# Performance work log

Hardware: AMD Instinct MI355X
Metric: run time of the kernel (lower is better)

The kernel has to match this reference:

```python
import jax, jax.numpy as jnp
import numpy as np

N_NODES = 50000
N_EDGES = 800000
IN_FEATS, HIDDEN, OUT = 256, 64, 32


def graph_conv(x, W, b, src, dst, n_nodes):
    # DGL GraphConv with norm='both': h = D_in^{-1/2} A D_out^{-1/2} (x W) + b
    ones = jnp.ones((src.shape[0],), dtype=x.dtype)
    deg_out = jax.ops.segment_sum(ones, src, num_segments=n_nodes)
    deg_in = jax.ops.segment_sum(ones, dst, num_segments=n_nodes)
    norm_out = jax.lax.rsqrt(jnp.maximum(deg_out, 1.0))  # [N]
    norm_in = jax.lax.rsqrt(jnp.maximum(deg_in, 1.0))    # [N]
    xw = x @ W                                # [N, out] dense transform first
    msg = (xw * norm_out[:, None])[src]       # [E, out] gather
    agg = jax.ops.segment_sum(msg, dst, num_segments=n_nodes)  # [N, out]
    return agg * norm_in[:, None] + b


def setup_inputs() -> dict:
    key = jax.random.key(0)
    ks = jax.random.split(key, 9)
    inputs = jax.random.normal(ks[0], (N_NODES, IN_FEATS), dtype=jnp.float32)
    src = jax.random.randint(ks[1], (N_EDGES,), 0, N_NODES)
    dst = jax.random.randint(ks[2], (N_EDGES,), 0, N_NODES)
    W1 = jax.random.normal(ks[3], (IN_FEATS, HIDDEN), dtype=jnp.float32) / np.sqrt(IN_FEATS)
    b1 = jnp.zeros((HIDDEN,), dtype=jnp.float32)
    W2 = jax.random.normal(ks[4], (HIDDEN, OUT), dtype=jnp.float32) / np.sqrt(HIDDEN)
    b2 = jnp.zeros((OUT,), dtype=jnp.float32)
    fc_w = jax.random.normal(ks[5], (N_NODES,), dtype=jnp.float32) / np.sqrt(N_NODES)
    fc_b = jnp.zeros((1,), dtype=jnp.float32)
    return {"inputs": inputs, "src": src, "dst": dst,
            "W1": W1, "b1": b1, "W2": W2, "b2": b2,
            "fc_w": fc_w, "fc_b": fc_b}


def reference(inputs, src, dst, W1, b1, W2, b2, fc_w, fc_b):
    g1 = jax.nn.relu(graph_conv(inputs, W1, b1, src, dst, N_NODES))  # [N, H]
    g2 = jax.nn.relu(graph_conv(g1, W2, b2, src, dst, N_NODES))      # [N, O]
    # fc(g2.t()): Linear(nodes, 1) on [O, N] -> [O, 1]
    out = jnp.einsum('no,n->o', g2, fc_w)[:, None] + fc_b
    return out
```

## Files before the change

kernel.cpp:

```cpp
#include <hip/hip_runtime.h>

#define N_NODES 50000
#define N_EDGES 800000
#define IN_FEATS 256
#define HIDDEN 64
#define OUTF 32
#define SCAN_BLOCKS 196

#define NSLICE 64
#define SLICE_E 12500
#define NRANGE 4
#define RANGE_N 12800
#define PSTRIDE 51200

#define HRANGE 2
#define HRANGE_N 25600

#define G32_BLOCKS 3125

typedef __attribute__((ext_vector_type(8))) short bf16x8;
typedef __attribute__((ext_vector_type(4))) float f32x4;
typedef unsigned short u16;

__device__ __forceinline__ unsigned f2bf_pk(float a, float b) {
    union { float f; unsigned u; } x, y;
    x.f = a; y.f = b;
    unsigned lo = x.u + 0x7FFFu + ((x.u >> 16) & 1u);
    unsigned hi = y.u + 0x7FFFu + ((y.u >> 16) & 1u);
    return (lo >> 16) | (hi & 0xFFFF0000u);
}
__device__ __forceinline__ u16 f2bf(float a) {
    union { float f; unsigned u; } x;
    x.f = a;
    return (u16)((x.u + 0x7FFFu + ((x.u >> 16) & 1u)) >> 16);
}
__device__ __forceinline__ float bflo(unsigned v) {
    union { unsigned u; float f; } x; x.u = v << 16; return x.f;
}
__device__ __forceinline__ float bfhi(unsigned v) {
    union { unsigned u; float f; } x; x.u = v & 0xFFFF0000u; return x.f;
}

__global__ __launch_bounds__(512) void hist_kernel(const int* __restrict__ src,
                                                   const int* __restrict__ dst,
                                                   unsigned char* __restrict__ partial) {
    __shared__ int h[HRANGE_N / 2];
    const int bid = blockIdx.x;
    const int which = bid & 1;
    const int r = (bid >> 1) & 1;
    const int s = bid >> 2;
    const int tid = threadIdx.x;
    const int lo = r * HRANGE_N;

    for (int i = tid; i < HRANGE_N / 2; i += 512) h[i] = 0;
    __syncthreads();

    const int* arr = which ? dst : src;
    const int e0 = s * SLICE_E;
    for (int j = tid; j < SLICE_E; j += 512) {
        int v = arr[e0 + j] - lo;
        if ((unsigned)v < HRANGE_N) atomicAdd(&h[v >> 1], 1 << ((v & 1) << 4));
    }
    __syncthreads();

    unsigned char* p = partial + (size_t)which * NSLICE * PSTRIDE + (size_t)s * PSTRIDE + lo;
    for (int i = tid; i < HRANGE_N / 2; i += 512) {
        int c = h[i];
        p[i * 2 + 0] = (unsigned char)(c & 0xFFFF);
        p[i * 2 + 1] = (unsigned char)((unsigned)c >> 16);
    }
}

__global__ __launch_bounds__(256) void reduce_scan_kernel(unsigned char* __restrict__ partial,
                                                          int* __restrict__ row_start,
                                                          int* __restrict__ block_sums,
                                                          float* __restrict__ norm_out,
                                                          float* __restrict__ norm_in) {
    __shared__ int sh[256];
    int i = blockIdx.x * 256 + threadIdx.x;
    int run = 0;
    if (i < N_NODES) {
        const unsigned char* ps = partial + i;
        unsigned char* pd = partial + (size_t)NSLICE * PSTRIDE + i;
        int so = 0;
#pragma unroll 8
        for (int s = 0; s < NSLICE; ++s) so += ps[(size_t)s * PSTRIDE];
        norm_out[i] = rsqrtf(fmaxf((float)so, 1.0f));
#pragma unroll 8
        for (int s = 0; s < NSLICE; ++s) {
            int c = pd[(size_t)s * PSTRIDE];
            pd[(size_t)s * PSTRIDE] = (unsigned char)run;
            run += c;
        }
        norm_in[i] = rsqrtf(fmaxf((float)run, 1.0f));
    }
    sh[threadIdx.x] = run;
    __syncthreads();
#pragma unroll
    for (int off = 1; off < 256; off <<= 1) {
        int t = (threadIdx.x >= off) ? sh[threadIdx.x - off] : 0;
        __syncthreads();
        sh[threadIdx.x] += t;
        __syncthreads();
    }
    if (i < N_NODES) row_start[i] = sh[threadIdx.x] - run;
    if (threadIdx.x == 255) block_sums[blockIdx.x] = sh[255];
}

__global__ __launch_bounds__(256) void scan3_kernel(int* __restrict__ row_start,
                                                    const int* __restrict__ block_sums) {
    __shared__ int s[256];
    int v = (threadIdx.x < SCAN_BLOCKS) ? block_sums[threadIdx.x] : 0;
    s[threadIdx.x] = v;
    __syncthreads();
#pragma unroll
    for (int off = 1; off < 256; off <<= 1) {
        int t = (threadIdx.x >= off) ? s[threadIdx.x - off] : 0;
        __syncthreads();
        s[threadIdx.x] += t;
        __syncthreads();
    }
    int base = (blockIdx.x == 0) ? 0 : s[blockIdx.x - 1];
    int i = blockIdx.x * 256 + threadIdx.x;
    if (i < N_NODES) row_start[i] += base;
    if (i == 0) row_start[N_NODES] = N_EDGES;
}

__global__ __launch_bounds__(512) void fill_csr_kernel(const int* __restrict__ src,
                                                       const int* __restrict__ dst,
                                                       const int* __restrict__ row_start,
                                                       const unsigned char* __restrict__ rel,
                                                       u16* __restrict__ csr16) {
    __shared__ int cur[RANGE_N];
    const int bid = blockIdx.x;
    const int r = bid & 3;
    const int s = bid >> 2;
    const int tid = threadIdx.x;
    const int lo = r * RANGE_N;

    const unsigned char* relp = rel + (size_t)s * PSTRIDE;
    for (int i = tid; i < RANGE_N; i += 512) {
        int node = lo + i;
        cur[i] = (node < N_NODES) ? row_start[node] + (int)relp[node] : 0;
    }
    __syncthreads();

    const int e0 = s * SLICE_E;
    for (int j = tid; j < SLICE_E; j += 512) {
        int d = dst[e0 + j] - lo;
        if ((unsigned)d < RANGE_N) {
            int pos = atomicAdd(&cur[d], 1);
            csr16[pos] = (u16)src[e0 + j];
        }
    }
}

#define AST 136
__global__ __launch_bounds__(256) void gemm1_kernel(const float* __restrict__ x,
                                                    const float* __restrict__ W1,
                                                    const float* __restrict__ norm_out,
                                                    u16* __restrict__ xw1) {
    __shared__ short As[64 * AST];
    __shared__ short Bt[64 * AST];
    const int tid = threadIdx.x;
    const int n0 = blockIdx.x * 64;

    const f32x4 zero4 = {0.f, 0.f, 0.f, 0.f};
    f32x4 acc[4] = {zero4, zero4, zero4, zero4};

    const int srow = tid >> 2;
    const int sseg = tid & 3;
    const int grow = n0 + srow;
    const bool grow_ok = grow < N_NODES;

    const int w = tid >> 6;
    const int l = tid & 63;

    for (int c = 0; c < 2; ++c) {
        if (c) __syncthreads();
        {
            const float* xp = x + (size_t)grow * IN_FEATS + c * 128 + sseg * 32;
            short* ap = As + srow * AST + sseg * 32;
#pragma unroll
            for (int j = 0; j < 8; ++j) {
                float4 v = make_float4(0.f, 0.f, 0.f, 0.f);
                if (grow_ok) v = *(const float4*)(xp + j * 4);
                unsigned p0 = f2bf_pk(v.x, v.y);
                unsigned p1 = f2bf_pk(v.z, v.w);
                *(uint2*)(ap + j * 4) = make_uint2(p0, p1);
            }
        }
        {
#pragma unroll
            for (int it = 0; it < 16; ++it) {
                int flat = tid + it * 256;
                int kp = flat >> 6;
                int col = flat & 63;
                int k = c * 128 + kp * 2;
                float w0 = W1[(size_t)k * HIDDEN + col];
                float w1 = W1[(size_t)(k + 1) * HIDDEN + col];
                *(unsigned*)(Bt + col * AST + kp * 2) = f2bf_pk(w0, w1);
            }
        }
        __syncthreads();

        const short* ap = As + (w * 16 + (l & 15)) * AST + (l >> 4) * 8;
        const short* bp = Bt + (l & 15) * AST + (l >> 4) * 8;
#pragma unroll
        for (int ks = 0; ks < 4; ++ks) {
            bf16x8 af = *(const bf16x8*)(ap + ks * 32);
#pragma unroll
            for (int ct = 0; ct < 4; ++ct) {
                bf16x8 bfv = *(const bf16x8*)(bp + ct * 16 * AST + ks * 32);
                acc[ct] = __builtin_amdgcn_mfma_f32_16x16x32_bf16(af, bfv, acc[ct], 0, 0, 0);
            }
        }
    }

    const int rbase = n0 + w * 16 + (l >> 4) * 4;
    const int cbase = l & 15;
#pragma unroll
    for (int j = 0; j < 4; ++j) {
        int row = rbase + j;
        if (row < N_NODES) {
            float nrm = norm_out[row];
            u16* orow = xw1 + (size_t)row * HIDDEN + cbase;
#pragma unroll
            for (int ct = 0; ct < 4; ++ct)
                orow[ct * 16] = f2bf(acc[ct][j] * nrm);
        }
    }
}

__global__ __launch_bounds__(256) void gather64_gemm2_kernel(const int* __restrict__ row_start,
                                                             const u16* __restrict__ csr16,
                                                             const u16* __restrict__ xw1,
                                                             const float* __restrict__ norm_in,
                                                             const float* __restrict__ b1,
                                                             const float* __restrict__ W2,
                                                             const float* __restrict__ norm_out,
                                                             u16* __restrict__ xw2) {
    __shared__ float gs[16][68];
    __shared__ float ws[HIDDEN * OUTF];
    const int tid = threadIdx.x;
#pragma unroll
    for (int i = 0; i < 8; ++i) ws[tid + i * 256] = W2[tid + i * 256];

    const int w = tid >> 6;
    const int l = tid & 63;
    const int p = l & 31;
    const int gsl = l >> 5;
    const int n0 = blockIdx.x * 16;

#pragma unroll
    for (int i4 = 0; i4 < 4; ++i4) {
        int nl = w * 4 + i4;
        int n = n0 + nl;
        int beg = row_start[n], end = row_start[n + 1];
        float ax = 0.f, ay = 0.f;
        int i = beg;
        for (; i + 8 <= end; i += 8) {
            int s0 = csr16[i + gsl];
            int s1 = csr16[i + 2 + gsl];
            int s2 = csr16[i + 4 + gsl];
            int s3 = csr16[i + 6 + gsl];
            unsigned v0 = *(const unsigned*)(xw1 + (size_t)s0 * 64 + 2 * p);
            unsigned v1 = *(const unsigned*)(xw1 + (size_t)s1 * 64 + 2 * p);
            unsigned v2 = *(const unsigned*)(xw1 + (size_t)s2 * 64 + 2 * p);
            unsigned v3 = *(const unsigned*)(xw1 + (size_t)s3 * 64 + 2 * p);
            ax += (bflo(v0) + bflo(v1)) + (bflo(v2) + bflo(v3));
            ay += (bfhi(v0) + bfhi(v1)) + (bfhi(v2) + bfhi(v3));
        }
        for (; i + 2 <= end; i += 2) {
            int s0 = csr16[i + gsl];
            unsigned v0 = *(const unsigned*)(xw1 + (size_t)s0 * 64 + 2 * p);
            ax += bflo(v0);
            ay += bfhi(v0);
        }
        if (i < end && gsl == 0) {
            int s0 = csr16[i];
            unsigned v0 = *(const unsigned*)(xw1 + (size_t)s0 * 64 + 2 * p);
            ax += bflo(v0);
            ay += bfhi(v0);
        }
        ax += __shfl_xor(ax, 32);
        ay += __shfl_xor(ay, 32);
        if (gsl == 0) {
            float nin = norm_in[n];
            gs[nl][2 * p]     = fmaxf(ax * nin + b1[2 * p], 0.f);
            gs[nl][2 * p + 1] = fmaxf(ay * nin + b1[2 * p + 1], 0.f);
        }
    }
    __syncthreads();

    const int o = tid & 31;
    const int r = tid >> 5;
    float a0 = 0.f, a1 = 0.f;
#pragma unroll 8
    for (int k = 0; k < 64; ++k) {
        float wv = ws[k * 32 + o];
        a0 += gs[r][k] * wv;
        a1 += gs[r + 8][k] * wv;
    }
    int row0 = n0 + r, row1 = n0 + r + 8;
    xw2[(size_t)row0 * 32 + o] = f2bf(a0 * norm_out[row0]);
    xw2[(size_t)row1 * 32 + o] = f2bf(a1 * norm_out[row1]);
}

__global__ __launch_bounds__(256) void gather32_kernel(const int* __restrict__ row_start,
                                                       const u16* __restrict__ csr16,
                                                       const u16* __restrict__ xw2,
                                                       const float* __restrict__ norm_in,
                                                       const float* __restrict__ b2,
                                                       const float* __restrict__ fc_w,
                                                       float* __restrict__ red) {
    __shared__ float sout[OUTF];
    const int tid = threadIdx.x;
    if (tid < OUTF) sout[tid] = 0.f;
    __syncthreads();

    const int w = tid >> 6;
    const int l = tid & 63;
    const int p = l & 15;
    const int gsl = l >> 4;
    const int n0 = blockIdx.x * 16;
    float tx = 0.f, ty = 0.f;

#pragma unroll
    for (int i4 = 0; i4 < 4; ++i4) {
        int n = n0 + w * 4 + i4;
        int beg = row_start[n], end = row_start[n + 1];
        float ax = 0.f, ay = 0.f;
        int i = beg;
        for (; i + 8 <= end; i += 8) {
            int s0 = csr16[i + gsl];
            int s1 = csr16[i + 4 + gsl];
            unsigned v0 = *(const unsigned*)(xw2 + (size_t)s0 * 32 + 2 * p);
            unsigned v1 = *(const unsigned*)(xw2 + (size_t)s1 * 32 + 2 * p);
            ax += bflo(v0) + bflo(v1);
            ay += bfhi(v0) + bfhi(v1);
        }
        for (; i + 4 <= end; i += 4) {
            int s0 = csr16[i + gsl];
            unsigned v0 = *(const unsigned*)(xw2 + (size_t)s0 * 32 + 2 * p);
            ax += bflo(v0);
            ay += bfhi(v0);
        }
        int t = end - i;
        if (gsl < t) {
            int s0 = csr16[i + gsl];
            unsigned v0 = *(const unsigned*)(xw2 + (size_t)s0 * 32 + 2 * p);
            ax += bflo(v0);
            ay += bfhi(v0);
        }
        ax += __shfl_xor(ax, 16); ax += __shfl_xor(ax, 32);
        ay += __shfl_xor(ay, 16); ay += __shfl_xor(ay, 32);
        if (gsl == 0) {
            float nin = norm_in[n], fw = fc_w[n];
            tx += fmaxf(ax * nin + b2[2 * p], 0.f) * fw;
            ty += fmaxf(ay * nin + b2[2 * p + 1], 0.f) * fw;
        }
    }
    if (gsl == 0) {
        atomicAdd(&sout[2 * p], tx);
        atomicAdd(&sout[2 * p + 1], ty);
    }
    __syncthreads();
    if (tid < OUTF) red[(size_t)blockIdx.x * OUTF + tid] = sout[tid];
}

__global__ __launch_bounds__(256) void reduce2_kernel(const float* __restrict__ red,
                                                      const float* __restrict__ fc_b,
                                                      float* __restrict__ out) {
    __shared__ float s[256];
    const int tid = threadIdx.x;
    const int o = blockIdx.x;
    float a = 0.f;
    for (int r = tid; r < G32_BLOCKS; r += 256)
        a += red[(size_t)r * OUTF + o];
    s[tid] = a;
    __syncthreads();
#pragma unroll
    for (int off = 128; off > 0; off >>= 1) {
        if (tid < off) s[tid] += s[tid + off];
        __syncthreads();
    }
    if (tid == 0) out[o] = s[0] + fc_b[0];
}

extern "C" void kernel_launch(void* const* d_in, const int* in_sizes, int n_in,
                              void* d_out, int out_size, void* d_ws, size_t ws_size,
                              hipStream_t stream) {
    const float* x    = (const float*)d_in[0];
    const int*   src  = (const int*)d_in[1];
    const int*   dst  = (const int*)d_in[2];
    const float* W1   = (const float*)d_in[3];
    const float* b1   = (const float*)d_in[4];
    const float* W2   = (const float*)d_in[5];
    const float* b2   = (const float*)d_in[6];
    const float* fc_w = (const float*)d_in[7];
    const float* fc_b = (const float*)d_in[8];
    float* out = (float*)d_out;

    u16* csr16      = (u16*)d_ws;
    int* row_start  = (int*)(csr16 + 800000);
    int* block_sums = row_start + 50004;
    u16* xw1_buf    = (u16*)(block_sums + 260);
    u16* xw2_buf    = xw1_buf + 3200000;
    float* norm_out = (float*)(xw2_buf + 1600000);
    float* norm_in  = norm_out + 50000;
    float* red      = norm_in + 50000;
    unsigned char* partial = (unsigned char*)(red + 100000);
    unsigned char* rel = partial + (size_t)NSLICE * PSTRIDE;

    hist_kernel<<<NSLICE * HRANGE * 2, 512, 0, stream>>>(src, dst, partial);
    reduce_scan_kernel<<<SCAN_BLOCKS, 256, 0, stream>>>(partial, row_start, block_sums,
                                                        norm_out, norm_in);
    scan3_kernel<<<SCAN_BLOCKS, 256, 0, stream>>>(row_start, block_sums);
    fill_csr_kernel<<<NSLICE * NRANGE, 512, 0, stream>>>(src, dst, row_start, rel, csr16);

    gemm1_kernel<<<(N_NODES + 63) / 64, 256, 0, stream>>>(x, W1, norm_out, xw1_buf);

    gather64_gemm2_kernel<<<N_NODES / 16, 256, 0, stream>>>(row_start, csr16, xw1_buf,
                                                            norm_in, b1, W2, norm_out,
                                                            xw2_buf);

    gather32_kernel<<<G32_BLOCKS, 256, 0, stream>>>(row_start, csr16, xw2_buf,
                                                    norm_in, b2, fc_w, red);
    reduce2_kernel<<<OUTF, 256, 0, stream>>>(red, fc_b, out);
}
```

Baseline: 138.6 us.

## Split layer-1 features into two 32-wide halves and gather each separately

```diff
diff --git a/kernel.cpp b/kernel.cpp
--- a/kernel.cpp
+++ b/kernel.cpp
@@ -17,6 +17,7 @@
 #define HRANGE_N 25600
 
 #define G32_BLOCKS 3125
+#define XH 1600000
 
 typedef __attribute__((ext_vector_type(8))) short bf16x8;
 typedef __attribute__((ext_vector_type(4))) float f32x4;
@@ -224,87 +225,112 @@
         int row = rbase + j;
         if (row < N_NODES) {
             float nrm = norm_out[row];
-            u16* orow = xw1 + (size_t)row * HIDDEN + cbase;
-#pragma unroll
-            for (int ct = 0; ct < 4; ++ct)
-                orow[ct * 16] = f2bf(acc[ct][j] * nrm);
-        }
-    }
-}
-
-__global__ __launch_bounds__(256) void gather64_gemm2_kernel(const int* __restrict__ row_start,
-                                                             const u16* __restrict__ csr16,
-                                                             const u16* __restrict__ xw1,
-                                                             const float* __restrict__ norm_in,
-                                                             const float* __restrict__ b1,
-                                                             const float* __restrict__ W2,
-                                                             const float* __restrict__ norm_out,
-                                                             u16* __restrict__ xw2) {
-    __shared__ float gs[16][68];
-    __shared__ float ws[HIDDEN * OUTF];
-    const int tid = threadIdx.x;
-#pragma unroll
-    for (int i = 0; i < 8; ++i) ws[tid + i * 256] = W2[tid + i * 256];
-
+#pragma unroll
+            for (int ct = 0; ct < 4; ++ct) {
+                int half = ct >> 1;
+                int fl = cbase + (ct & 1) * 16;
+                xw1[(size_t)half * XH + (size_t)row * 32 + fl] = f2bf(acc[ct][j] * nrm);
+            }
+        }
+    }
+}
+
+__global__ __launch_bounds__(256) void gather64h_kernel(const int* __restrict__ row_start,
+                                                        const u16* __restrict__ csr16,
+                                                        const u16* __restrict__ xw1,
+                                                        const float* __restrict__ norm_in,
+                                                        const float* __restrict__ b1,
+                                                        u16* __restrict__ g1,
+                                                        int h) {
+    const int tid = threadIdx.x;
     const int w = tid >> 6;
     const int l = tid & 63;
-    const int p = l & 31;
-    const int gsl = l >> 5;
+    const int p = l & 15;
+    const int gsl = l >> 4;
     const int n0 = blockIdx.x * 16;
+    const u16* xh = xw1 + (size_t)h * XH;
+    u16* gh = g1 + (size_t)h * XH;
+    const float bx = b1[h * 32 + 2 * p];
+    const float by = b1[h * 32 + 2 * p + 1];
 
 #pragma unroll
     for (int i4 = 0; i4 < 4; ++i4) {
-        int nl = w * 4 + i4;
-        int n = n0 + nl;
+        int n = n0 + w * 4 + i4;
         int beg = row_start[n], end = row_start[n + 1];
         float ax = 0.f, ay = 0.f;
         int i = beg;
-        for (; i + 8 <= end; i += 8) {
-            int s0 = csr16[i + gsl];
-            int s1 = csr16[i + 2 + gsl];
-            int s2 = csr16[i + 4 + gsl];
-            int s3 = csr16[i + 6 + gsl];
-            unsigned v0 = *(const unsigned*)(xw1 + (size_t)s0 * 64 + 2 * p);
-            unsigned v1 = *(const unsigned*)(xw1 + (size_t)s1 * 64 + 2 * p);
-            unsigned v2 = *(const unsigned*)(xw1 + (size_t)s2 * 64 + 2 * p);
-            unsigned v3 = *(const unsigned*)(xw1 + (size_t)s3 * 64 + 2 * p);
+        for (; i + 16 <= end; i += 16) {
+            int s0 = __builtin_nontemporal_load(csr16 + i + gsl);
+            int s1 = __builtin_nontemporal_load(csr16 + i + 4 + gsl);
+            int s2 = __builtin_nontemporal_load(csr16 + i + 8 + gsl);
+            int s3 = __builtin_nontemporal_load(csr16 + i + 12 + gsl);
+            unsigned v0 = *(const unsigned*)(xh + (size_t)s0 * 32 + 2 * p);
+            unsigned v1 = *(const unsigned*)(xh + (size_t)s1 * 32 + 2 * p);
+            unsigned v2 = *(const unsigned*)(xh + (size_t)s2 * 32 + 2 * p);
+            unsigned v3 = *(const unsigned*)(xh + (size_t)s3 * 32 + 2 * p);
             ax += (bflo(v0) + bflo(v1)) + (bflo(v2) + bflo(v3));
             ay += (bfhi(v0) + bfhi(v1)) + (bfhi(v2) + bfhi(v3));
         }
-        for (; i + 2 <= end; i += 2) {
-            int s0 = csr16[i + gsl];
-            unsigned v0 = *(const unsigned*)(xw1 + (size_t)s0 * 64 + 2 * p);
+        for (; i + 8 <= end; i += 8) {
+            int s0 = __builtin_nontemporal_load(csr16 + i + gsl);
+            int s1 = __builtin_nontemporal_load(csr16 + i + 4 + gsl);
+            unsigned v0 = *(const unsigned*)(xh + (size_t)s0 * 32 + 2 * p);
+            unsigned v1 = *(const unsigned*)(xh + (size_t)s1 * 32 + 2 * p);
+            ax += bflo(v0) + bflo(v1);
+            ay += bfhi(v0) + bfhi(v1);
+        }
+        for (; i + 4 <= end; i += 4) {
+            int s0 = __builtin_nontemporal_load(csr16 + i + gsl);
+            unsigned v0 = *(const unsigned*)(xh + (size_t)s0 * 32 + 2 * p);
             ax += bflo(v0);
             ay += bfhi(v0);
         }
-        if (i < end && gsl == 0) {
-            int s0 = csr16[i];
-            unsigned v0 = *(const unsigned*)(xw1 + (size_t)s0 * 64 + 2 * p);
+        int t = end - i;
+        if (gsl < t) {
+            int s0 = __builtin_nontemporal_load(csr16 + i + gsl);
+            unsigned v0 = *(const unsigned*)(xh + (size_t)s0 * 32 + 2 * p);
             ax += bflo(v0);
             ay += bfhi(v0);
         }
-        ax += __shfl_xor(ax, 32);
-        ay += __shfl_xor(ay, 32);
+        ax += __shfl_xor(ax, 16); ax += __shfl_xor(ax, 32);
+        ay += __shfl_xor(ay, 16); ay += __shfl_xor(ay, 32);
         if (gsl == 0) {
             float nin = norm_in[n];
-            gs[nl][2 * p]     = fmaxf(ax * nin + b1[2 * p], 0.f);
-            gs[nl][2 * p + 1] = fmaxf(ay * nin + b1[2 * p + 1], 0.f);
-        }
+            float rx = fmaxf(ax * nin + bx, 0.f);
+            float ry = fmaxf(ay * nin + by, 0.f);
+            __builtin_nontemporal_store(f2bf_pk(rx, ry),
+                                        (unsigned*)(gh + (size_t)n * 32 + 2 * p));
+        }
+    }
+}
+
+__global__ __launch_bounds__(256) void gemm2_kernel(const u16* __restrict__ g1,
+                                                    const float* __restrict__ W2,
+                                                    const float* __restrict__ norm_out,
+                                                    u16* __restrict__ xw2) {
+    __shared__ float gs[8][64];
+    __shared__ float ws[HIDDEN * OUTF];
+    const int tid = threadIdx.x;
+    const int n0 = blockIdx.x * 8;
+
+#pragma unroll
+    for (int i = 0; i < 8; ++i) ws[tid + i * 256] = W2[tid + i * 256];
+    {
+        int r = tid >> 5, oo = tid & 31;
+        int h = oo >> 4, pp = oo & 15;
+        unsigned v = *(const unsigned*)(g1 + (size_t)h * XH + (size_t)(n0 + r) * 32 + 2 * pp);
+        gs[r][h * 32 + 2 * pp]     = bflo(v);
+        gs[r][h * 32 + 2 * pp + 1] = bfhi(v);
     }
     __syncthreads();
 
     const int o = tid & 31;
     const int r = tid >> 5;
-    float a0 = 0.f, a1 = 0.f;
+    float acc = 0.f;
 #pragma unroll 8
-    for (int k = 0; k < 64; ++k) {
-        float wv = ws[k * 32 + o];
-        a0 += gs[r][k] * wv;
-        a1 += gs[r + 8][k] * wv;
-    }
-    int row0 = n0 + r, row1 = n0 + r + 8;
-    xw2[(size_t)row0 * 32 + o] = f2bf(a0 * norm_out[row0]);
-    xw2[(size_t)row1 * 32 + o] = f2bf(a1 * norm_out[row1]);
+    for (int k = 0; k < 64; ++k) acc += gs[r][k] * ws[k * 32 + o];
+    int row = n0 + r;
+    xw2[(size_t)row * 32 + o] = f2bf(acc * norm_out[row]);
 }
 
 __global__ __launch_bounds__(256) void gather32_kernel(const int* __restrict__ row_start,
@@ -332,6 +358,18 @@
         int beg = row_start[n], end = row_start[n + 1];
         float ax = 0.f, ay = 0.f;
         int i = beg;
+        for (; i + 16 <= end; i += 16) {
+            int s0 = csr16[i + gsl];
+            int s1 = csr16[i + 4 + gsl];
+            int s2 = csr16[i + 8 + gsl];
+            int s3 = csr16[i + 12 + gsl];
+            unsigned v0 = *(const unsigned*)(xw2 + (size_t)s0 * 32 + 2 * p);
+            unsigned v1 = *(const unsigned*)(xw2 + (size_t)s1 * 32 + 2 * p);
+            unsigned v2 = *(const unsigned*)(xw2 + (size_t)s2 * 32 + 2 * p);
+            unsigned v3 = *(const unsigned*)(xw2 + (size_t)s3 * 32 + 2 * p);
+            ax += (bflo(v0) + bflo(v1)) + (bflo(v2) + bflo(v3));
+            ay += (bfhi(v0) + bfhi(v1)) + (bfhi(v2) + bfhi(v3));
+        }
         for (; i + 8 <= end; i += 8) {
             int s0 = csr16[i + gsl];
             int s1 = csr16[i + 4 + gsl];
@@ -406,8 +444,9 @@
     int* row_start  = (int*)(csr16 + 800000);
     int* block_sums = row_start + 50004;
     u16* xw1_buf    = (u16*)(block_sums + 260);
-    u16* xw2_buf    = xw1_buf + 3200000;
-    float* norm_out = (float*)(xw2_buf + 1600000);
+    u16* xw2_buf    = xw1_buf + 2 * XH;
+    u16* g1_buf     = xw2_buf + 1600000;
+    float* norm_out = (float*)(g1_buf + 2 * XH);
     float* norm_in  = norm_out + 50000;
     float* red      = norm_in + 50000;
     unsigned char* partial = (unsigned char*)(red + 100000);
@@ -421,9 +460,12 @@
 
     gemm1_kernel<<<(N_NODES + 63) / 64, 256, 0, stream>>>(x, W1, norm_out, xw1_buf);
 
-    gather64_gemm2_kernel<<<N_NODES / 16, 256, 0, stream>>>(row_start, csr16, xw1_buf,
-                                                            norm_in, b1, W2, norm_out,
-                                                            xw2_buf);
+    gather64h_kernel<<<G32_BLOCKS, 256, 0, stream>>>(row_start, csr16, xw1_buf,
+                                                     norm_in, b1, g1_buf, 0);
+    gather64h_kernel<<<G32_BLOCKS, 256, 0, stream>>>(row_start, csr16, xw1_buf,
+                                                     norm_in, b1, g1_buf, 1);
+
+    gemm2_kernel<<<N_NODES / 8, 256, 0, stream>>>(g1_buf, W2, norm_out, xw2_buf);
 
     gather32_kernel<<<G32_BLOCKS, 256, 0, stream>>>(row_start, csr16, xw2_buf,
                                                     norm_in, b2, fc_w, red);
```

New measurement: 164.0 us. +18.3%, slower.
